# Optimization experiments

Hardware: AMD Instinct MI355X
Metric: run time of the kernel (lower is better)

The kernel has to match this reference:

```python
import jax, jax.numpy as jnp
import numpy as np

HEADS, DH = 4, 128
SCALE = DH ** -0.5
EPS = 1e-5  # torch LayerNorm/BatchNorm default eps


def _ln(h, g, b):
    mu = jnp.mean(h, axis=-1, keepdims=True)
    v = jnp.mean((h - mu) ** 2, axis=-1, keepdims=True)
    return (h - mu) / jnp.sqrt(v + EPS) * g + b


def _bn_eval(z, g, b, rm, rv):
    # eval-mode BatchNorm1d on (B, C, T)
    return (z - rm[None, :, None]) / jnp.sqrt(rv[None, :, None] + EPS) * g[None, :, None] + b[None, :, None]


def setup_inputs() -> dict:
    key = jax.random.key(0)
    ks = iter(jax.random.split(key, 40))
    B, N, T, D, C, L = 32, 10, 256, 1024, 512, 2
    rn = lambda shape, s=0.02: jax.random.normal(next(ks), shape, jnp.float32) * s
    inp = {"x": jax.random.normal(next(ks), (B, N, T, D), jnp.float32)}
    # Temporal: Conv1d(1024 -> 512, k=3, pad=1)
    inp["W_emb"] = rn((C, D, 3)); inp["b_emb"] = jnp.zeros((C,), jnp.float32)
    # Transformer(512, depth=2, heads=4, dim_head=128, mlp_dim=512)
    inp["tf_ln1_g"] = jnp.ones((L, C)); inp["tf_ln1_b"] = jnp.zeros((L, C))
    inp["tf_Wqkv"] = rn((L, C, 3 * HEADS * DH))
    inp["tf_Wo"] = rn((L, HEADS * DH, C)); inp["tf_bo"] = jnp.zeros((L, C))
    inp["tf_ln2_g"] = jnp.ones((L, C)); inp["tf_ln2_b"] = jnp.zeros((L, C))
    inp["tf_W1"] = rn((L, C, 512)); inp["tf_b1"] = jnp.zeros((L, 512))
    inp["tf_W2"] = rn((L, 512, C)); inp["tf_b2"] = jnp.zeros((L, C))
    # NormalHead: 512 -> 512//16=32 -> 512//32=16 -> 1, all k=1
    C1, C2 = C // 16, C // 32
    inp["c1_W"] = rn((C1, C, 1)); inp["c1_b"] = jnp.zeros((C1,))
    inp["bn1_g"] = jnp.ones((C1,)); inp["bn1_b"] = jnp.zeros((C1,))
    inp["bn1_rm"] = rn((C1,), 0.1)
    inp["bn1_rv"] = jax.random.uniform(next(ks), (C1,), jnp.float32, 0.5, 1.5)
    inp["c2_W"] = rn((C2, C1, 1)); inp["c2_b"] = jnp.zeros((C2,))
    inp["bn2_g"] = jnp.ones((C2,)); inp["bn2_b"] = jnp.zeros((C2,))
    inp["bn2_rm"] = rn((C2,), 0.1)
    inp["bn2_rv"] = jax.random.uniform(next(ks), (C2,), jnp.float32, 0.5, 1.5)
    inp["c3_W"] = rn((1, C2, 1)); inp["c3_b"] = jnp.zeros((1,))
    return inp


def reference(x, W_emb, b_emb, tf_ln1_g, tf_ln1_b, tf_Wqkv, tf_Wo, tf_bo, tf_ln2_g, tf_ln2_b, tf_W1, tf_b1, tf_W2, tf_b2, c1_W, c1_b, bn1_g, bn1_b, bn1_rm, bn1_rv, c2_W, c2_b, bn2_g, bn2_b, bn2_rm, bn2_rv, c3_W, c3_b):
    b, n, t, d = x.shape
    h = x.reshape(b * n, t, d)
    # Temporal embedding: Conv1d(k=3, pad=1) over time, then ReLU  -> (bn, t, 512)
    z = jax.lax.conv_general_dilated(h.transpose(0, 2, 1), W_emb, (1,), [(1, 1)],
                                     dimension_numbers=("NCH", "OIH", "NCH"))
    h = jax.nn.relu(z + b_emb[None, :, None]).transpose(0, 2, 1)
    bn_ = b * n
    # self-attention transformer (pre-norm, residual)
    for l in range(tf_Wqkv.shape[0]):
        u = _ln(h, tf_ln1_g[l], tf_ln1_b[l])
        q, k, v = jnp.split(u @ tf_Wqkv[l], 3, axis=-1)
        sh = lambda a: a.reshape(bn_, t, HEADS, DH).transpose(0, 2, 1, 3)
        attn = jax.nn.softmax(jnp.einsum("bhqd,bhkd->bhqk", sh(q), sh(k)) * SCALE, axis=-1)
        o = jnp.einsum("bhqk,bhkd->bhqd", attn, sh(v)).transpose(0, 2, 1, 3).reshape(bn_, t, HEADS * DH)
        h = h + o @ tf_Wo[l] + tf_bo[l]
        u = _ln(h, tf_ln2_g[l], tf_ln2_b[l])
        h = h + jax.nn.gelu(u @ tf_W1[l] + tf_b1[l], approximate=False) @ tf_W2[l] + tf_b2[l]
    # NormalHead on (bn, 512, t); k=1 convs as einsums
    f = h.transpose(0, 2, 1)
    x1 = jnp.einsum("bct,oc->bot", f, c1_W[:, :, 0]) + c1_b[None, :, None]
    x2 = jnp.einsum("bct,oc->bot", jax.nn.relu(_bn_eval(x1, bn1_g, bn1_b, bn1_rm, bn1_rv)), c2_W[:, :, 0]) + c2_b[None, :, None]
    scores = jax.nn.sigmoid(jnp.einsum("bct,oc->bot", jax.nn.relu(_bn_eval(x2, bn2_g, bn2_b, bn2_rm, bn2_rv)), c3_W[:, :, 0]) + c3_b[None, :, None])
    normal_scores = scores.reshape(b, n, t).mean(axis=1)  # (b, t)
    # Mahalanobis distance to BN running stats (note: raw running_var, no eps, as in source)
    d1 = jnp.sqrt(jnp.sum((x1 - bn1_rm[None, :, None]) ** 2 / bn1_rv[None, :, None], axis=1)).reshape(b, n, t).mean(axis=1)
    d2 = jnp.sqrt(jnp.sum((x2 - bn2_rm[None, :, None]) ** 2 / bn2_rv[None, :, None], axis=1)).reshape(b, n, t).mean(axis=1)
    return (d1 + d2) * normal_scores
```

## Files before the change

kernel.cpp:

```cpp
#include <hip/hip_runtime.h>
#include <math.h>

#define T_SEQ 256
#define C_DIM 512
#define D_DIM 1024
#define BN_TOT 320
#define NHEAD 4
#define DHEAD 128
#define QKV_N 1536
#define EPS 1e-5f
#define ATT_SCALE 0.08838834764831845f

typedef unsigned short u16;
typedef unsigned int u32;
typedef __attribute__((ext_vector_type(8))) short bf16x8;
typedef __attribute__((ext_vector_type(4))) float f32x4;

__device__ __forceinline__ u16 f2bf(float f) {
  union { float f; u32 u; } v; v.f = f;
  u32 r = v.u + 0x7fffu + ((v.u >> 16) & 1u);
  return (u16)(r >> 16);
}

__device__ __forceinline__ void gload_lds16(const u16* g, u16* l) {
  __builtin_amdgcn_global_load_lds((const __attribute__((address_space(1))) u32*)g,
                                   (__attribute__((address_space(3))) u32*)l, 16, 0, 0);
}

__global__ void convert_x(const float* __restrict__ x, u16* __restrict__ xpad) {
  size_t i4 = ((size_t)blockIdx.x * 256 + threadIdx.x) * 4;
  if (i4 >= (size_t)BN_TOT * 258 * 1024) return;
  size_t row = i4 >> 10; int col = (int)(i4 & 1023);
  int bn = (int)(row / 258), tr = (int)(row % 258);
  ushort4 o;
  if (tr == 0 || tr == 257) {
    o.x = 0; o.y = 0; o.z = 0; o.w = 0;
  } else {
    float4 v = *(const float4*)&x[((size_t)bn * 256 + tr - 1) * 1024 + col];
    o.x = f2bf(v.x); o.y = f2bf(v.y); o.z = f2bf(v.z); o.w = f2bf(v.w);
  }
  *(ushort4*)&xpad[i4] = o;
}

__global__ void prep_wct(const float* __restrict__ Wemb, u16* __restrict__ Wct) {
  int idx = blockIdx.x * 256 + threadIdx.x;
  if (idx >= 3 * C_DIM * D_DIM) return;
  int d = idx & 1023;
  int c = (idx >> 10) & 511;
  int s = idx >> 19;
  Wct[idx] = f2bf(Wemb[(c * D_DIM + d) * 3 + s]);
}

__launch_bounds__(256)
__global__ void transpose_w(const float* __restrict__ src, u16* __restrict__ dst, int K, int N) {
  __shared__ float t[32][33];
  int tid = threadIdx.x;
  int n0 = blockIdx.x * 32, k0 = blockIdx.y * 32;
  int r = tid >> 3, c4 = (tid & 7) * 4;
  float4 v = *(const float4*)&src[(size_t)(k0 + r) * N + n0 + c4];
  t[r][c4 + 0] = v.x; t[r][c4 + 1] = v.y; t[r][c4 + 2] = v.z; t[r][c4 + 3] = v.w;
  __syncthreads();
  ushort4 o;
  o.x = f2bf(t[c4 + 0][r]);
  o.y = f2bf(t[c4 + 1][r]);
  o.z = f2bf(t[c4 + 2][r]);
  o.w = f2bf(t[c4 + 3][r]);
  *(ushort4*)&dst[(size_t)(n0 + r) * K + k0 + c4] = o;
}

__global__ void prep_c1t(const float* __restrict__ c1W, float* __restrict__ Wt) {
  int idx = blockIdx.x * 256 + threadIdx.x;
  if (idx >= C_DIM * 32) return;
  int n = idx & 31;
  int k = idx >> 5;
  Wt[idx] = c1W[n * C_DIM + k];
}

template <int S, int EPI>
__launch_bounds__(256)
__global__ void gemm_mfma(const u16* __restrict__ A, int lda, int aRowsPerZ,
                          const u16* __restrict__ Bt, size_t bShift, int K,
                          float* __restrict__ C, u16* __restrict__ Cbf,
                          const float* __restrict__ bias, int N, int cRowsPerZ) {
  __shared__ __align__(16) float smem_f[64 * 132];
  u16* lds = (u16*)smem_f;
  u16* Alds = lds;
  u16* Blds = lds + 8192;
  float (*ldsT)[132] = (float (*)[132])smem_f;

  const int tid = threadIdx.x;
  const int lane = tid & 63;
  const int wave = tid >> 6;
  const int wm = wave >> 1, wn = wave & 1;
  const int quad = lane >> 4;
  const int l15 = lane & 15;
  const int srow = lane >> 3;
  const int scol = ((lane & 7) ^ srow) * 8;
  const int xk = (l15 & 7) * 8;

  unsigned gx = gridDim.x, gy = gridDim.y, gz = gridDim.z;
  unsigned orig = (blockIdx.z * gy + blockIdx.y) * gx + blockIdx.x;
  unsigned nwg = gx * gy * gz;
  unsigned wg = orig;
  if ((nwg & 7u) == 0u) wg = (orig & 7u) * (nwg >> 3) + (orig >> 3);
  unsigned bx = wg % gx;
  unsigned tmp = wg / gx;
  unsigned by = tmp % gy;
  unsigned bz = tmp / gy;

  const int n0 = bx * 128;
  const int arow0 = bz * aRowsPerZ + by * 128;
  const int crow0 = bz * cRowsPerZ + by * 128;

  f32x4 acc[4][4] = {};

  for (int s = 0; s < S; ++s) {
    const u16* Ab = A + ((size_t)arow0 + s) * (size_t)lda;
    const u16* Bb = Bt + (size_t)s * bShift;
    for (int k0 = 0; k0 < K; k0 += 64) {
#pragma unroll
      for (int c = 0; c < 4; ++c) {
        int chunk = wave * 4 + c;
        gload_lds16(Ab + (size_t)(chunk * 8 + srow) * lda + k0 + scol,
                    Alds + chunk * 512);
      }
#pragma unroll
      for (int c = 0; c < 4; ++c) {
        int chunk = wave * 4 + c;
        gload_lds16(Bb + (size_t)(n0 + chunk * 8 + srow) * K + k0 + scol,
                    Blds + chunk * 512);
      }
      __syncthreads();
#pragma unroll
      for (int kk = 0; kk < 64; kk += 32) {
        bf16x8 af[4], bfr[4];
#pragma unroll
        for (int mt = 0; mt < 4; ++mt)
          af[mt] = *(const bf16x8*)&Alds[(wm * 64 + mt * 16 + l15) * 64 + ((kk + quad * 8) ^ xk)];
#pragma unroll
        for (int nt = 0; nt < 4; ++nt)
          bfr[nt] = *(const bf16x8*)&Blds[(wn * 64 + nt * 16 + l15) * 64 + ((kk + quad * 8) ^ xk)];
#pragma unroll
        for (int mt = 0; mt < 4; ++mt)
#pragma unroll
          for (int nt = 0; nt < 4; ++nt)
            acc[mt][nt] = __builtin_amdgcn_mfma_f32_16x16x32_bf16(af[mt], bfr[nt], acc[mt][nt], 0, 0, 0);
      }
      __syncthreads();
    }
  }

  const int rgrp = tid >> 5;
  const int c4 = (tid & 31) * 4;
  const int gcol = n0 + c4;
  float4 bias4 = make_float4(0.f, 0.f, 0.f, 0.f);
  if constexpr (EPI == 1 || EPI == 2 || EPI == 3) bias4 = *(const float4*)&bias[gcol];

#pragma unroll
  for (int p = 0; p < 2; ++p) {
    if (wm == p) {
#pragma unroll
      for (int mt = 0; mt < 4; ++mt)
#pragma unroll
        for (int nt = 0; nt < 4; ++nt)
#pragma unroll
          for (int r = 0; r < 4; ++r)
            ldsT[mt * 16 + quad * 4 + r][wn * 64 + nt * 16 + l15] = acc[mt][nt][r];
    }
    __syncthreads();
#pragma unroll
    for (int j = 0; j < 8; ++j) {
      int lrow = rgrp * 8 + j;
      size_t grow = (size_t)crow0 + p * 64 + lrow;
      float4 v = *(const float4*)&ldsT[lrow][c4];
      if constexpr (EPI == 0) {
        *(float4*)&C[grow * N + gcol] = v;
      } else if constexpr (EPI == 1) {
        float4 c = *(const float4*)&C[grow * N + gcol];
        c.x += v.x + bias4.x; c.y += v.y + bias4.y;
        c.z += v.z + bias4.z; c.w += v.w + bias4.w;
        *(float4*)&C[grow * N + gcol] = c;
      } else if constexpr (EPI == 2) {
        float t0 = v.x + bias4.x, t1 = v.y + bias4.y, t2 = v.z + bias4.z, t3 = v.w + bias4.w;
        ushort4 o;
        o.x = f2bf(t0 * 0.5f * (1.f + erff(t0 * 0.70710678118f)));
        o.y = f2bf(t1 * 0.5f * (1.f + erff(t1 * 0.70710678118f)));
        o.z = f2bf(t2 * 0.5f * (1.f + erff(t2 * 0.70710678118f)));
        o.w = f2bf(t3 * 0.5f * (1.f + erff(t3 * 0.70710678118f)));
        *(ushort4*)&Cbf[grow * N + gcol] = o;
      } else if constexpr (EPI == 3) {
        float4 c;
        c.x = fmaxf(v.x + bias4.x, 0.f); c.y = fmaxf(v.y + bias4.y, 0.f);
        c.z = fmaxf(v.z + bias4.z, 0.f); c.w = fmaxf(v.w + bias4.w, 0.f);
        *(float4*)&C[grow * N + gcol] = c;
      } else {
        ushort4 o;
        o.x = f2bf(v.x); o.y = f2bf(v.y); o.z = f2bf(v.z); o.w = f2bf(v.w);
        *(ushort4*)&Cbf[grow * N + gcol] = o;
      }
    }
    __syncthreads();
  }
}

template <int NT, int EPI>
__launch_bounds__(256)
__global__ void gemm_f32(const float* __restrict__ A, const float* __restrict__ B,
                         float* __restrict__ C, const float* __restrict__ bias,
                         int M, int N, int K) {
  __shared__ __align__(16) float As[16][68];
  __shared__ __align__(16) float Bs[16][NT + 4];
  int tid = threadIdx.x;
  int tx = tid & 15, ty = tid >> 4;
  int n0 = blockIdx.x * NT, m0 = blockIdx.y * 64;
  constexpr int TN = NT / 16;
  float acc[4][TN] = {};
  int arow = tid >> 2, akg = (tid & 3) * 4;
  int bk, bng;
  if (NT == 64) { bk = tid >> 4; bng = (tid & 15) * 4; }
  else          { bk = tid >> 3; bng = (tid & 7) * 4; }
  bool bload = (NT == 64) || (tid < 128);
  const float* Ap = A + (size_t)(m0 + arow) * K + akg;
  const float* Bp = B + (size_t)bk * N + n0 + bng;
  for (int k0 = 0; k0 < K; k0 += 16) {
    float4 av = *(const float4*)(Ap + k0);
    float4 bv = make_float4(0.f, 0.f, 0.f, 0.f);
    if (bload) bv = *(const float4*)(Bp + (size_t)k0 * N);
    __syncthreads();
    As[akg + 0][arow] = av.x; As[akg + 1][arow] = av.y;
    As[akg + 2][arow] = av.z; As[akg + 3][arow] = av.w;
    if (bload) *(float4*)&Bs[bk][bng] = bv;
    __syncthreads();
#pragma unroll
    for (int k = 0; k < 16; ++k) {
      float4 a4 = *(const float4*)&As[k][ty * 4];
      float a[4] = {a4.x, a4.y, a4.z, a4.w};
      float b[TN];
#pragma unroll
      for (int j = 0; j < TN; j++) b[j] = Bs[k][tx * TN + j];
#pragma unroll
      for (int i = 0; i < 4; i++)
#pragma unroll
        for (int j = 0; j < TN; j++) acc[i][j] = fmaf(a[i], b[j], acc[i][j]);
    }
  }
#pragma unroll
  for (int i = 0; i < 4; i++) {
    size_t row = m0 + ty * 4 + i;
    float* Cp = C + row * (size_t)N + n0 + tx * TN;
#pragma unroll
    for (int j = 0; j < TN; j++) {
      float v = acc[i][j];
      if (EPI >= 1) v += bias[n0 + tx * TN + j];
      Cp[j] = v;
    }
  }
}

__launch_bounds__(256)
__global__ void ln_kernel(const float* __restrict__ h, const float* __restrict__ g,
                          const float* __restrict__ b, u16* __restrict__ u) {
  int row = blockIdx.x * 4 + (threadIdx.x >> 6);
  int lane = threadIdx.x & 63;
  const float* hp = h + (size_t)row * C_DIM + lane * 8;
  float4 a0 = *(const float4*)hp;
  float4 a1 = *(const float4*)(hp + 4);
  float s = a0.x + a0.y + a0.z + a0.w + a1.x + a1.y + a1.z + a1.w;
#pragma unroll
  for (int o = 32; o > 0; o >>= 1) s += __shfl_xor(s, o);
  float mu = s * (1.f / 512.f);
  float d[8] = {a0.x - mu, a0.y - mu, a0.z - mu, a0.w - mu,
                a1.x - mu, a1.y - mu, a1.z - mu, a1.w - mu};
  float q = 0.f;
#pragma unroll
  for (int j = 0; j < 8; ++j) q += d[j] * d[j];
#pragma unroll
  for (int o = 32; o > 0; o >>= 1) q += __shfl_xor(q, o);
  float rs = rsqrtf(q * (1.f / 512.f) + EPS);
  const float* gp = g + lane * 8;
  const float* bp = b + lane * 8;
  float4 g0 = *(const float4*)gp, g1 = *(const float4*)(gp + 4);
  float4 b0 = *(const float4*)bp, b1 = *(const float4*)(bp + 4);
  float gv[8] = {g0.x, g0.y, g0.z, g0.w, g1.x, g1.y, g1.z, g1.w};
  float bv[8] = {b0.x, b0.y, b0.z, b0.w, b1.x, b1.y, b1.z, b1.w};
  ushort4 o0, o1;
  o0.x = f2bf(d[0] * rs * gv[0] + bv[0]);
  o0.y = f2bf(d[1] * rs * gv[1] + bv[1]);
  o0.z = f2bf(d[2] * rs * gv[2] + bv[2]);
  o0.w = f2bf(d[3] * rs * gv[3] + bv[3]);
  o1.x = f2bf(d[4] * rs * gv[4] + bv[4]);
  o1.y = f2bf(d[5] * rs * gv[5] + bv[5]);
  o1.z = f2bf(d[6] * rs * gv[6] + bv[6]);
  o1.w = f2bf(d[7] * rs * gv[7] + bv[7]);
  u16* up = u + (size_t)row * C_DIM + lane * 8;
  *(ushort4*)up = o0;
  *(ushort4*)(up + 4) = o1;
}

__launch_bounds__(512, 2)
__global__ void attn_mfma(const u16* __restrict__ qkv, u16* __restrict__ o) {
  __shared__ u16 Ks[64 * 136];
  __shared__ u32 Vt32[128 * 44];
  __shared__ u16 Ps[8][32 * 80];

  const int tid = threadIdx.x;
  const int lane = tid & 63, wave = tid >> 6;
  const int quad = lane >> 4, l15 = lane & 15;
  const int hh = blockIdx.x, bl = blockIdx.y;
  const u16* base = qkv + (size_t)bl * T_SEQ * QKV_N;

  bf16x8 qf[2][4];
#pragma unroll
  for (int mi = 0; mi < 2; mi++) {
    int row = wave * 32 + mi * 16 + l15;
    const u16* qp = base + (size_t)row * QKV_N + hh * DHEAD + quad * 8;
#pragma unroll
    for (int k0 = 0; k0 < 4; k0++)
      qf[mi][k0] = *(const bf16x8*)(qp + k0 * 32);
  }

  f32x4 oa[2][8] = {};
  float mrow[2][4], lrow[2][4];
#pragma unroll
  for (int mi = 0; mi < 2; mi++)
#pragma unroll
    for (int r = 0; r < 4; r++) { mrow[mi][r] = -1e30f; lrow[mi][r] = 0.f; }

  for (int kt = 0; kt < 4; kt++) {
    __syncthreads();
    {
      int kk = tid >> 3, dbase = (tid & 7) * 16;
      const u16* kp = base + (size_t)(kt * 64 + kk) * QKV_N + C_DIM + hh * DHEAD + dbase;
      uint4 a = *(const uint4*)kp;
      uint4 b = *(const uint4*)(kp + 8);
      *(uint4*)&Ks[kk * 136 + dbase] = a;
      *(uint4*)&Ks[kk * 136 + dbase + 8] = b;
    }
    {
      int kkp = tid >> 4, dbase = (tid & 15) * 8;
      const u16* vp = base + (size_t)(kt * 64 + kkp * 2) * QKV_N + 2 * C_DIM + hh * DHEAD + dbase;
      union { uint4 u; u16 h[8]; } va, vb;
      va.u = *(const uint4*)vp;
      vb.u = *(const uint4*)(vp + QKV_N);
#pragma unroll
      for (int j = 0; j < 8; j++)
        Vt32[(dbase + j) * 44 + kkp] = (u32)va.h[j] | ((u32)vb.h[j] << 16);
    }
    __syncthreads();

    f32x4 sa[2][4] = {};
#pragma unroll
    for (int k0 = 0; k0 < 4; k0++) {
      bf16x8 kf[4];
#pragma unroll
      for (int ni = 0; ni < 4; ni++)
        kf[ni] = *(const bf16x8*)&Ks[(ni * 16 + l15) * 136 + k0 * 32 + quad * 8];
      __builtin_amdgcn_s_setprio(1);
#pragma unroll
      for (int mi = 0; mi < 2; mi++)
#pragma unroll
        for (int ni = 0; ni < 4; ni++)
          sa[mi][ni] = __builtin_amdgcn_mfma_f32_16x16x32_bf16(qf[mi][k0], kf[ni], sa[mi][ni], 0, 0, 0);
      __builtin_amdgcn_s_setprio(0);
    }

#pragma unroll
    for (int mi = 0; mi < 2; mi++) {
#pragma unroll
      for (int r = 0; r < 4; r++) {
        float mx = fmaxf(fmaxf(sa[mi][0][r], sa[mi][1][r]), fmaxf(sa[mi][2][r], sa[mi][3][r]));
        mx = fmaxf(mx, __shfl_xor(mx, 1));
        mx = fmaxf(mx, __shfl_xor(mx, 2));
        mx = fmaxf(mx, __shfl_xor(mx, 4));
        mx = fmaxf(mx, __shfl_xor(mx, 8));
        mx *= ATT_SCALE;
        float mnew = fmaxf(mrow[mi][r], mx);
        float alpha = __expf(mrow[mi][r] - mnew);
        mrow[mi][r] = mnew;
        float rs = 0.f;
#pragma unroll
        for (int ni = 0; ni < 4; ni++) {
          float p = __expf(sa[mi][ni][r] * ATT_SCALE - mnew);
          rs += p;
          Ps[wave][(mi * 16 + quad * 4 + r) * 80 + ni * 16 + l15] = f2bf(p);
        }
        rs += __shfl_xor(rs, 1);
        rs += __shfl_xor(rs, 2);
        rs += __shfl_xor(rs, 4);
        rs += __shfl_xor(rs, 8);
        lrow[mi][r] = lrow[mi][r] * alpha + rs;
#pragma unroll
        for (int nj = 0; nj < 8; nj++) oa[mi][nj][r] *= alpha;
      }
    }

#pragma unroll
    for (int k0 = 0; k0 < 2; k0++) {
      bf16x8 pf[2];
#pragma unroll
      for (int mi = 0; mi < 2; mi++)
        pf[mi] = *(const bf16x8*)&Ps[wave][(mi * 16 + l15) * 80 + k0 * 32 + quad * 8];
      __builtin_amdgcn_s_setprio(1);
#pragma unroll
      for (int nj = 0; nj < 8; nj++) {
        bf16x8 vf = *(const bf16x8*)&Vt32[(nj * 16 + l15) * 44 + k0 * 16 + quad * 4];
#pragma unroll
        for (int mi = 0; mi < 2; mi++)
          oa[mi][nj] = __builtin_amdgcn_mfma_f32_16x16x32_bf16(pf[mi], vf, oa[mi][nj], 0, 0, 0);
      }
      __builtin_amdgcn_s_setprio(0);
    }
  }

#pragma unroll
  for (int mi = 0; mi < 2; mi++) {
#pragma unroll
    for (int r = 0; r < 4; r++) {
      int row = wave * 32 + mi * 16 + quad * 4 + r;
      float inv = 1.f / lrow[mi][r];
      u16* op = o + ((size_t)bl * T_SEQ + row) * C_DIM + hh * DHEAD + l15;
#pragma unroll
      for (int nj = 0; nj < 8; nj++)
        op[nj * 16] = f2bf(oa[mi][nj][r] * inv);
    }
  }
}

__global__ void head_kernel(const float* __restrict__ x1,
                            const float* __restrict__ bn1g, const float* __restrict__ bn1b,
                            const float* __restrict__ bn1rm, const float* __restrict__ bn1rv,
                            const float* __restrict__ c2W, const float* __restrict__ c2b,
                            const float* __restrict__ bn2g, const float* __restrict__ bn2b,
                            const float* __restrict__ bn2rm, const float* __restrict__ bn2rv,
                            const float* __restrict__ c3W, const float* __restrict__ c3b,
                            float* __restrict__ d1a, float* __restrict__ d2a, float* __restrict__ sca) {
  int r = blockIdx.x * 256 + threadIdx.x;
  if (r >= BN_TOT * T_SEQ) return;
  const float* xp = x1 + (size_t)r * 32;
  float y[32];
  float d1 = 0.f;
#pragma unroll
  for (int oc = 0; oc < 32; oc++) {
    float v = xp[oc];
    float dm = v - bn1rm[oc];
    d1 += dm * dm / bn1rv[oc];
    float t = dm * rsqrtf(bn1rv[oc] + EPS) * bn1g[oc] + bn1b[oc];
    y[oc] = fmaxf(t, 0.f);
  }
  float d2 = 0.f, sacc = 0.f;
#pragma unroll
  for (int o2 = 0; o2 < 16; o2++) {
    float s2 = 0.f;
#pragma unroll
    for (int oc = 0; oc < 32; oc++) s2 = fmaf(y[oc], c2W[o2 * 32 + oc], s2);
    s2 += c2b[o2];
    float dm = s2 - bn2rm[o2];
    d2 += dm * dm / bn2rv[o2];
    float t = dm * rsqrtf(bn2rv[o2] + EPS) * bn2g[o2] + bn2b[o2];
    t = fmaxf(t, 0.f);
    sacc = fmaf(t, c3W[o2], sacc);
  }
  float sc = 1.f / (1.f + expf(-(sacc + c3b[0])));
  d1a[r] = sqrtf(d1);
  d2a[r] = sqrtf(d2);
  sca[r] = sc;
}

__global__ void reduce_kernel(const float* __restrict__ d1a, const float* __restrict__ d2a,
                              const float* __restrict__ sca, float* __restrict__ out) {
  int idx = blockIdx.x * 256 + threadIdx.x;
  if (idx >= 32 * T_SEQ) return;
  int b = idx >> 8, t = idx & 255;
  float s1 = 0.f, s2 = 0.f, ss = 0.f;
  for (int n = 0; n < 10; n++) {
    int r = (b * 10 + n) * T_SEQ + t;
    s1 += d1a[r];
    s2 += d2a[r];
    ss += sca[r];
  }
  out[idx] = (s1 + s2) * ss * 0.01f;
}

extern "C" void kernel_launch(void* const* d_in, const int* in_sizes, int n_in,
                              void* d_out, int out_size, void* d_ws, size_t ws_size,
                              hipStream_t stream) {
  const float* x     = (const float*)d_in[0];
  const float* Wemb  = (const float*)d_in[1];
  const float* bemb  = (const float*)d_in[2];
  const float* ln1g  = (const float*)d_in[3];
  const float* ln1b  = (const float*)d_in[4];
  const float* Wqkv  = (const float*)d_in[5];
  const float* Wo    = (const float*)d_in[6];
  const float* bo    = (const float*)d_in[7];
  const float* ln2g  = (const float*)d_in[8];
  const float* ln2b  = (const float*)d_in[9];
  const float* W1    = (const float*)d_in[10];
  const float* b1    = (const float*)d_in[11];
  const float* W2    = (const float*)d_in[12];
  const float* b2    = (const float*)d_in[13];
  const float* c1W   = (const float*)d_in[14];
  const float* c1b   = (const float*)d_in[15];
  const float* bn1g  = (const float*)d_in[16];
  const float* bn1b  = (const float*)d_in[17];
  const float* bn1rm = (const float*)d_in[18];
  const float* bn1rv = (const float*)d_in[19];
  const float* c2W   = (const float*)d_in[20];
  const float* c2b   = (const float*)d_in[21];
  const float* bn2g  = (const float*)d_in[22];
  const float* bn2b  = (const float*)d_in[23];
  const float* bn2rm = (const float*)d_in[24];
  const float* bn2rv = (const float*)d_in[25];
  const float* c3W   = (const float*)d_in[26];
  const float* c3b   = (const float*)d_in[27];

  char* w = (char*)d_ws;
  size_t off = 0;
  auto alloc = [&](size_t nbytes) {
    void* p = (void*)(w + off);
    off += (nbytes + 255) & ~(size_t)255;
    return p;
  };
  float* h      = (float*)alloc((size_t)BN_TOT * T_SEQ * C_DIM * 4);
  u16*   u_bf   = (u16*)  alloc((size_t)BN_TOT * T_SEQ * C_DIM * 2);
  u16*   scratch= (u16*)  alloc((size_t)BN_TOT * T_SEQ * QKV_N * 2);
  u16*   Wct    = (u16*)  alloc((size_t)3 * C_DIM * D_DIM * 2);
  u16*   Wqkvt  = (u16*)  alloc((size_t)2 * QKV_N * C_DIM * 2);
  u16*   Wot    = (u16*)  alloc((size_t)2 * C_DIM * C_DIM * 2);
  u16*   W1t    = (u16*)  alloc((size_t)2 * C_DIM * C_DIM * 2);
  u16*   W2t    = (u16*)  alloc((size_t)2 * C_DIM * C_DIM * 2);
  float* Wc1t   = (float*)alloc((size_t)C_DIM * 32 * 4);
  float* x1     = (float*)alloc((size_t)BN_TOT * T_SEQ * 32 * 4);
  float* d1a    = (float*)alloc((size_t)BN_TOT * T_SEQ * 4);
  float* d2a    = (float*)alloc((size_t)BN_TOT * T_SEQ * 4);
  float* sca    = (float*)alloc((size_t)BN_TOT * T_SEQ * 4);
  u16* xpad  = scratch;
  u16* qkvbf = scratch;
  u16* midbf = scratch;

  {
    size_t nx4 = (size_t)BN_TOT * 258 * 1024 / 4;
    convert_x<<<(unsigned)((nx4 + 255) / 256), 256, 0, stream>>>(x, xpad);
  }
  prep_wct<<<(3 * C_DIM * D_DIM + 255) / 256, 256, 0, stream>>>(Wemb, Wct);
  for (int l = 0; l < 2; ++l) {
    transpose_w<<<dim3(QKV_N / 32, C_DIM / 32), 256, 0, stream>>>(
        Wqkv + (size_t)l * C_DIM * QKV_N, Wqkvt + (size_t)l * QKV_N * C_DIM, C_DIM, QKV_N);
    transpose_w<<<dim3(C_DIM / 32, C_DIM / 32), 256, 0, stream>>>(
        Wo + (size_t)l * C_DIM * C_DIM, Wot + (size_t)l * C_DIM * C_DIM, C_DIM, C_DIM);
    transpose_w<<<dim3(C_DIM / 32, C_DIM / 32), 256, 0, stream>>>(
        W1 + (size_t)l * C_DIM * C_DIM, W1t + (size_t)l * C_DIM * C_DIM, C_DIM, C_DIM);
    transpose_w<<<dim3(C_DIM / 32, C_DIM / 32), 256, 0, stream>>>(
        W2 + (size_t)l * C_DIM * C_DIM, W2t + (size_t)l * C_DIM * C_DIM, C_DIM, C_DIM);
  }
  prep_c1t<<<(C_DIM * 32 + 255) / 256, 256, 0, stream>>>(c1W, Wc1t);

  gemm_mfma<3, 3><<<dim3(C_DIM / 128, 2, BN_TOT), 256, 0, stream>>>(
      xpad, 1024, 258, Wct, (size_t)C_DIM * D_DIM, D_DIM, h, nullptr, bemb, C_DIM, 256);

  for (int l = 0; l < 2; ++l) {
    ln_kernel<<<BN_TOT * T_SEQ / 4, 256, 0, stream>>>(h, ln1g + l * C_DIM, ln1b + l * C_DIM, u_bf);
    gemm_mfma<1, 4><<<dim3(QKV_N / 128, 640, 1), 256, 0, stream>>>(
        u_bf, C_DIM, 0, Wqkvt + (size_t)l * QKV_N * C_DIM, 0, C_DIM,
        nullptr, qkvbf, nullptr, QKV_N, 0);
    attn_mfma<<<dim3(NHEAD, BN_TOT), 512, 0, stream>>>(qkvbf, u_bf);
    gemm_mfma<1, 1><<<dim3(C_DIM / 128, 640, 1), 256, 0, stream>>>(
        u_bf, C_DIM, 0, Wot + (size_t)l * C_DIM * C_DIM, 0, C_DIM, h, nullptr, bo + l * C_DIM, C_DIM, 0);
    ln_kernel<<<BN_TOT * T_SEQ / 4, 256, 0, stream>>>(h, ln2g + l * C_DIM, ln2b + l * C_DIM, u_bf);
    gemm_mfma<1, 2><<<dim3(C_DIM / 128, 640, 1), 256, 0, stream>>>(
        u_bf, C_DIM, 0, W1t + (size_t)l * C_DIM * C_DIM, 0, C_DIM, nullptr, midbf, b1 + l * C_DIM, C_DIM, 0);
    gemm_mfma<1, 1><<<dim3(C_DIM / 128, 640, 1), 256, 0, stream>>>(
        midbf, C_DIM, 0, W2t + (size_t)l * C_DIM * C_DIM, 0, C_DIM, h, nullptr, b2 + l * C_DIM, C_DIM, 0);
  }

  gemm_f32<32, 1><<<dim3(1, 81920 / 64), 256, 0, stream>>>(h, Wc1t, x1, c1b, 81920, 32, C_DIM);
  head_kernel<<<(BN_TOT * T_SEQ + 255) / 256, 256, 0, stream>>>(
      x1, bn1g, bn1b, bn1rm, bn1rv, c2W, c2b, bn2g, bn2b, bn2rm, bn2rv, c3W, c3b, d1a, d2a, sca);
  reduce_kernel<<<32, 256, 0, stream>>>(d1a, d2a, sca, (float*)d_out);
}
```

Baseline: 2.460 ms.

## Double-buffer LDS tiles in MFMA GEMM to overlap global loads with compute

Restructures the GEMM main loop into a two-stage software pipeline. The next K-tile is loaded into an alternate LDS buffer while MFMAs run on the current one, with one barrier per step instead of two. This aims to hide global-to-LDS latency behind matrix math. LDS use doubles to 64KB per block, which may reduce occupancy.

```diff
diff --git a/kernel.cpp b/kernel.cpp
--- a/kernel.cpp
+++ b/kernel.cpp
@@ -82,11 +82,8 @@
                           const u16* __restrict__ Bt, size_t bShift, int K,
                           float* __restrict__ C, u16* __restrict__ Cbf,
                           const float* __restrict__ bias, int N, int cRowsPerZ) {
-  __shared__ __align__(16) float smem_f[64 * 132];
-  u16* lds = (u16*)smem_f;
-  u16* Alds = lds;
-  u16* Blds = lds + 8192;
-  float (*ldsT)[132] = (float (*)[132])smem_f;
+  __shared__ __align__(16) u16 lds_all[2 * 16384];
+  float (*ldsT)[132] = (float (*)[132])lds_all;
 
   const int tid = threadIdx.x;
   const int lane = tid & 63;
@@ -112,43 +109,68 @@
   const int arow0 = bz * aRowsPerZ + by * 128;
   const int crow0 = bz * cRowsPerZ + by * 128;
 
+  const int ksteps = K >> 6;
+  const int nt = S * ksteps;
+
   f32x4 acc[4][4] = {};
 
-  for (int s = 0; s < S; ++s) {
-    const u16* Ab = A + ((size_t)arow0 + s) * (size_t)lda;
-    const u16* Bb = Bt + (size_t)s * bShift;
-    for (int k0 = 0; k0 < K; k0 += 64) {
-#pragma unroll
-      for (int c = 0; c < 4; ++c) {
-        int chunk = wave * 4 + c;
-        gload_lds16(Ab + (size_t)(chunk * 8 + srow) * lda + k0 + scol,
-                    Alds + chunk * 512);
-      }
-#pragma unroll
-      for (int c = 0; c < 4; ++c) {
-        int chunk = wave * 4 + c;
-        gload_lds16(Bb + (size_t)(n0 + chunk * 8 + srow) * K + k0 + scol,
-                    Blds + chunk * 512);
-      }
-      __syncthreads();
-#pragma unroll
-      for (int kk = 0; kk < 64; kk += 32) {
-        bf16x8 af[4], bfr[4];
-#pragma unroll
-        for (int mt = 0; mt < 4; ++mt)
-          af[mt] = *(const bf16x8*)&Alds[(wm * 64 + mt * 16 + l15) * 64 + ((kk + quad * 8) ^ xk)];
-#pragma unroll
-        for (int nt = 0; nt < 4; ++nt)
-          bfr[nt] = *(const bf16x8*)&Blds[(wn * 64 + nt * 16 + l15) * 64 + ((kk + quad * 8) ^ xk)];
-#pragma unroll
-        for (int mt = 0; mt < 4; ++mt)
-#pragma unroll
-          for (int nt = 0; nt < 4; ++nt)
-            acc[mt][nt] = __builtin_amdgcn_mfma_f32_16x16x32_bf16(af[mt], bfr[nt], acc[mt][nt], 0, 0, 0);
-      }
-      __syncthreads();
-    }
-  }
+  auto stage = [&](int buf, int t) {
+    int s = (S == 1) ? 0 : (t / ksteps);
+    int k0 = (S == 1) ? (t << 6) : ((t - s * ksteps) << 6);
+    const u16* Ab = A + ((size_t)arow0 + s) * (size_t)lda + k0;
+    const u16* Bb = Bt + (size_t)s * bShift + k0;
+    u16* Al = lds_all + buf * 16384;
+    u16* Bl = Al + 8192;
+#pragma unroll
+    for (int c = 0; c < 4; ++c) {
+      int chunk = wave * 4 + c;
+      gload_lds16(Ab + (size_t)(chunk * 8 + srow) * lda + scol, Al + chunk * 512);
+    }
+#pragma unroll
+    for (int c = 0; c < 4; ++c) {
+      int chunk = wave * 4 + c;
+      gload_lds16(Bb + (size_t)(n0 + chunk * 8 + srow) * K + scol, Bl + chunk * 512);
+    }
+  };
+
+  auto compute = [&](int buf) {
+    const u16* Al = lds_all + buf * 16384;
+    const u16* Bl = Al + 8192;
+#pragma unroll
+    for (int kk = 0; kk < 64; kk += 32) {
+      bf16x8 af[4], bfr[4];
+#pragma unroll
+      for (int mt = 0; mt < 4; ++mt)
+        af[mt] = *(const bf16x8*)&Al[(wm * 64 + mt * 16 + l15) * 64 + ((kk + quad * 8) ^ xk)];
+#pragma unroll
+      for (int nt2 = 0; nt2 < 4; ++nt2)
+        bfr[nt2] = *(const bf16x8*)&Bl[(wn * 64 + nt2 * 16 + l15) * 64 + ((kk + quad * 8) ^ xk)];
+#pragma unroll
+      for (int mt = 0; mt < 4; ++mt)
+#pragma unroll
+        for (int nt2 = 0; nt2 < 4; ++nt2)
+          acc[mt][nt2] = __builtin_amdgcn_mfma_f32_16x16x32_bf16(af[mt], bfr[nt2], acc[mt][nt2], 0, 0, 0);
+    }
+  };
+
+  stage(0, 0);
+  asm volatile("s_waitcnt vmcnt(0)" ::: "memory");
+  __builtin_amdgcn_s_barrier();
+  __builtin_amdgcn_sched_barrier(0);
+
+  int cur = 0;
+  for (int t = 0; t < nt - 1; ++t) {
+    stage(cur ^ 1, t + 1);
+    compute(cur);
+    __builtin_amdgcn_sched_barrier(0);
+    asm volatile("s_waitcnt vmcnt(0)" ::: "memory");
+    __builtin_amdgcn_s_barrier();
+    __builtin_amdgcn_sched_barrier(0);
+    cur ^= 1;
+  }
+  compute(cur);
+
+  __syncthreads();
 
   const int rgrp = tid >> 5;
   const int c4 = (tid & 31) * 4;
@@ -162,10 +184,10 @@
 #pragma unroll
       for (int mt = 0; mt < 4; ++mt)
 #pragma unroll
-        for (int nt = 0; nt < 4; ++nt)
+        for (int nt2 = 0; nt2 < 4; ++nt2)
 #pragma unroll
           for (int r = 0; r < 4; ++r)
-            ldsT[mt * 16 + quad * 4 + r][wn * 64 + nt * 16 + l15] = acc[mt][nt][r];
+            ldsT[mt * 16 + quad * 4 + r][wn * 64 + nt2 * 16 + l15] = acc[mt][nt2][r];
     }
     __syncthreads();
 #pragma unroll
```

Result: faster. 2.381 ms (-3.2%).
